# Performance work log

Hardware: AMD Instinct MI355X
Metric: run time of the kernel (lower is better)

Reference implementation:

```python
import jax, jax.numpy as jnp
import numpy as np

H = 16
HD = 128
ROPE_BASE = 10000.0

def _rope_cos_sin(T, dtype):
    inv_freq = 1.0 / (ROPE_BASE ** (jnp.arange(0, HD, 2, dtype=jnp.float32) / HD))  # [HD/2]
    pos = jnp.arange(T, dtype=jnp.float32)
    freqs = pos[:, None] * inv_freq[None, :]  # [T, HD/2]
    return jnp.cos(freqs).astype(dtype), jnp.sin(freqs).astype(dtype)

def _apply_rotary(x, cos, sin):
    # x: [B,H,T,HD]; cos/sin: [T,HD/2]
    x1, x2 = x[..., : HD // 2], x[..., HD // 2 :]
    c = cos[None, None, :, :]
    s = sin[None, None, :, :]
    return jnp.concatenate([x1 * c - x2 * s, x1 * s + x2 * c], axis=-1)

def setup_inputs() -> dict:
    key = jax.random.key(0)
    ks = jax.random.split(key, 5)
    B, T, D = 2, 2048, 2048
    x = jax.random.normal(ks[0], (B, T, D), dtype=jnp.float32)
    Wqkv = jax.random.normal(ks[1], (3 * D, D), dtype=jnp.float32) * (D ** -0.5)
    bqkv = jax.random.normal(ks[2], (3 * D,), dtype=jnp.float32) * 0.02
    Wo = jax.random.normal(ks[3], (D, D), dtype=jnp.float32) * (D ** -0.5)
    bo = jax.random.normal(ks[4], (D,), dtype=jnp.float32) * 0.02
    # causal mask: True = masked (future positions)
    mask = jnp.triu(jnp.ones((T, T), dtype=bool), k=1)[None, None, :, :]
    return {"x": x, "Wqkv": Wqkv, "bqkv": bqkv, "Wo": Wo, "bo": bo, "mask": mask}

def reference(x, Wqkv, bqkv, Wo, bo, mask):
    B, T, D = x.shape
    qkv = x @ Wqkv.T + bqkv  # [B,T,3D]
    q, k, v = jnp.split(qkv, 3, axis=-1)
    def to_heads(t):
        return t.reshape(B, T, H, HD).transpose(0, 2, 1, 3)  # [B,H,T,HD]
    q, k, v = to_heads(q), to_heads(k), to_heads(v)
    cos, sin = _rope_cos_sin(T, x.dtype)
    q = _apply_rotary(q, cos, sin)
    k = _apply_rotary(k, cos, sin)
    scale = HD ** 0.5
    attn = jnp.einsum('bhqd,bhkd->bhqk', q, k) / scale
    neg = -jnp.finfo(x.dtype).max
    attn = jnp.where(mask, neg, attn)
    w = jax.nn.softmax(attn, axis=-1)
    out = jnp.einsum('bhqk,bhkd->bhqd', w, v)  # [B,H,T,HD]
    out = out.transpose(0, 2, 1, 3).reshape(B, T, H * HD)
    return out @ Wo.T + bo
```

## Files before the change

kernel.cpp:

```cpp
#include <hip/hip_runtime.h>
#include <hip/hip_bf16.h>
#include <cstdint>

typedef __bf16 bf16;
typedef __bf16 bf16x8 __attribute__((ext_vector_type(8)));
typedef float  f32x4  __attribute__((ext_vector_type(4)));

#define B_   2
#define T_   2048
#define D_   2048
#define H_   16
#define HD_  128

typedef __attribute__((address_space(3))) void       lds_void;
typedef __attribute__((address_space(1))) const void gbl_void;
__device__ __forceinline__ void glds16(const bf16* g, bf16* l) {
    __builtin_amdgcn_global_load_lds((gbl_void*)g, (lds_void*)l, 16, 0, 0);
}

__device__ __forceinline__ ushort4 cvt4(const float4 v) {
    union { bf16 h[4]; ushort4 u; } pk;
    pk.h[0] = (bf16)v.x; pk.h[1] = (bf16)v.y;
    pk.h[2] = (bf16)v.z; pk.h[3] = (bf16)v.w;
    return pk.u;
}

__global__ __launch_bounds__(256) void convert_xw_kernel(
    const float* __restrict__ x, const float* __restrict__ wqkv,
    bf16* __restrict__ xb, bf16* __restrict__ wqkvb)
{
    const int NX = (B_ * T_ * D_) / 4;
    const int NT = NX + (3 * D_ * D_) / 4;
    for (int g = blockIdx.x * blockDim.x + threadIdx.x; g < NT;
         g += gridDim.x * blockDim.x) {
        if (g < NX) ((ushort4*)xb)[g]      = cvt4(((const float4*)x)[g]);
        else        ((ushort4*)wqkvb)[g-NX] = cvt4(((const float4*)wqkv)[g-NX]);
    }
}

__global__ __launch_bounds__(256) void convert_wo_kernel(
    const float* __restrict__ wo, bf16* __restrict__ wob)
{
    const int N = (D_ * D_) / 4;
    for (int g = blockIdx.x * blockDim.x + threadIdx.x; g < N;
         g += gridDim.x * blockDim.x)
        ((ushort4*)wob)[g] = cvt4(((const float4*)wo)[g]);
}

__device__ __forceinline__ void gemm_core_glds(
    const bf16* __restrict__ A, const bf16* __restrict__ W, int K,
    int bm, int bn, int tid, f32x4 (&acc)[4][4],
    bf16* lds_a, bf16* lds_b)
{
    const int lane = tid & 63, quad = lane >> 4, lcol = lane & 15;
    const int wave = tid >> 6;
    const int wm = (wave >> 1) * 64, wn2 = (wave & 1) * 32;
    const int sw = lcol & 7;
    const int sr = tid >> 3, pc = tid & 7;
    const int sc = (pc ^ (sr & 7)) * 8;
    const bf16* abase = A + (size_t)(bm * 128 + sr) * K + sc;
    const bf16* bbase = W + (size_t)(bn * 128 + sr) * K + sc;
    bf16* la = lds_a + sr * 64 + pc * 8;
    bf16* lb = lds_b + sr * 64 + pc * 8;

    for (int k0 = 0; k0 < K; k0 += 64) {
        __syncthreads();
#pragma unroll
        for (int p = 0; p < 4; p++) {
            glds16(abase + k0 + (size_t)32 * p * K, la + 2048 * p);
            glds16(bbase + k0 + (size_t)32 * p * K, lb + 2048 * p);
        }
        __syncthreads();
#pragma unroll
        for (int kk = 0; kk < 2; kk++) {
            bf16x8 af[4], bfr[4];
#pragma unroll
            for (int i = 0; i < 4; i++)
                af[i] = *(const bf16x8*)&lds_a[(wm + i * 16 + lcol) * 64 +
                                               (((kk * 4 + quad) ^ sw) * 8)];
#pragma unroll
            for (int j = 0; j < 4; j++) {
                const int row = wn2 + (j & 1) * 16 + (j >> 1) * 64 + lcol;
                bfr[j] = *(const bf16x8*)&lds_b[row * 64 +
                                                (((kk * 4 + quad) ^ sw) * 8)];
            }
#pragma unroll
            for (int i = 0; i < 4; i++)
#pragma unroll
                for (int j = 0; j < 4; j++)
                    acc[i][j] = __builtin_amdgcn_mfma_f32_16x16x32_bf16(af[i], bfr[j], acc[i][j], 0, 0, 0);
        }
    }
}

__global__ __launch_bounds__(256) void qkv_gemm_kernel(
    const bf16* __restrict__ xb, const bf16* __restrict__ wqkvb,
    const float* __restrict__ bias,
    bf16* __restrict__ qh, bf16* __restrict__ kh, bf16* __restrict__ vT)
{
    __shared__ bf16 lds_a[128 * 64];
    __shared__ bf16 lds_b[128 * 64];
    const int tid = threadIdx.x;
    const int bm = blockIdx.y, bn = blockIdx.x;
    const int lane = tid & 63, quad = lane >> 4, lcol = lane & 15;
    const int wave = tid >> 6;
    const int wm = (wave >> 1) * 64, wn2 = (wave & 1) * 32;

    f32x4 acc[4][4];
    const f32x4 z = {0.f, 0.f, 0.f, 0.f};
#pragma unroll
    for (int i = 0; i < 4; i++)
#pragma unroll
        for (int j = 0; j < 4; j++) acc[i][j] = z;

    gemm_core_glds(xb, wqkvb, D_, bm, bn, tid, acc, lds_a, lds_b);

    const int n0 = bn * 128;
    const int part = bn / 16;
    const int h = bn & 15;
    const int mb0 = bm * 128 + wm;

    if (part < 2) {
        bf16* dst = (part == 0) ? qh : kh;
#pragma unroll
        for (int i = 0; i < 4; i++) {
#pragma unroll
            for (int jp = 0; jp < 2; jp++) {
                const int d1 = wn2 + jp * 16 + lcol;
                const float invf = __expf(-0.14391156831212787f * (float)d1);
                const float b1 = bias[n0 + d1];
                const float b2 = bias[n0 + d1 + 64];
#pragma unroll
                for (int r = 0; r < 4; r++) {
                    const int m = mb0 + i * 16 + quad * 4 + r;
                    const int bb = m >> 11, t = m & (T_ - 1);
                    const float x1 = acc[i][jp][r] + b1;
                    const float x2 = acc[i][jp + 2][r] + b2;
                    float s, c;
                    __sincosf((float)t * invf, &s, &c);
                    const size_t rowo = ((size_t)(bb * H_ + h) * T_ + t) * HD_;
                    dst[rowo + d1]      = (bf16)(x1 * c - x2 * s);
                    dst[rowo + d1 + 64] = (bf16)(x1 * s + x2 * c);
                }
            }
        }
    } else {
        const int bb = mb0 >> 11, t64 = mb0 & (T_ - 1);
        const int bh = bb * H_ + h;
#pragma unroll
        for (int j = 0; j < 4; j++) {
            const int d = wn2 + (j & 1) * 16 + (j >> 1) * 64 + lcol;
            const float bv = bias[n0 + d];
            bf16* vdst = &vT[((size_t)bh * HD_ + d) * T_ + t64];
#pragma unroll
            for (int r = 0; r < 4; r++) {
                union { bf16 hh[4]; ushort4 u; } pk;
#pragma unroll
                for (int i = 0; i < 4; i++) pk.hh[i] = (bf16)(acc[i][j][r] + bv);
                *(ushort4*)&vdst[(quad * 4 + r) * 4] = pk.u;
            }
        }
    }
}

__global__ __launch_bounds__(256) void attn_kernel(
    const bf16* __restrict__ qh, const bf16* __restrict__ kh,
    const bf16* __restrict__ vT, bf16* __restrict__ ctx)
{
    __shared__ bf16 lds_k[2][64 * 128];
    __shared__ bf16 lds_v[2][128 * 64];
    __shared__ bf16 lds_p[64 * 64];
    const int tid = threadIdx.x;
    const int id = blockIdx.x;
    const int bh = id & 31;
    const int qp = id >> 5;
    const int qtA = 31 - qp;
    const int qtB = qp;
    const int ktA = qtA + 1;
    const int lane = tid & 63, quad = lane >> 4, lcol = lane & 15;
    const int wave = tid >> 6;
    const int wq0 = wave * 16;
    const float scale2 = 0.08838834764831845f * 1.4426950408889634f;
    const int b = bh >> 4, h = bh & 15;

    const bf16* kbase = kh + (size_t)bh * T_ * HD_;
    const bf16* vbase = vT + (size_t)bh * HD_ * T_;

    const int ksrow = tid >> 4;
    const bf16* kstage = kbase + (size_t)ksrow * HD_ + (((tid & 15) ^ ksrow) << 3);
    const int vsd = tid >> 3;
    const bf16* vstage = vbase + (size_t)vsd * T_ + (((tid & 7) ^ (vsd & 7)) << 3);

    int qt_cur = qtA;
    int q0 = qtA * 64;

    bf16x8 qf[4];
    auto load_q = [&](int q0_) {
#pragma unroll
        for (int kk = 0; kk < 4; kk++)
            qf[kk] = *(const bf16x8*)&qh[((size_t)bh * T_ + q0_ + wq0 + lcol) * HD_ +
                                         kk * 32 + quad * 8];
    };
    load_q(q0);

    f32x4 o[8];
    const f32x4 z = {0.f, 0.f, 0.f, 0.f};
#pragma unroll
    for (int jd = 0; jd < 8; jd++) o[jd] = z;
    float l_part[4] = {0.f, 0.f, 0.f, 0.f};

    auto do_epilogue = [&](int q0_) {
        float inv_l[4];
#pragma unroll
        for (int r = 0; r < 4; r++) {
            float rs = l_part[r];
#pragma unroll
            for (int off = 1; off < 16; off <<= 1)
                rs += __shfl_xor(rs, off);
            inv_l[r] = 1.0f / rs;
        }
#pragma unroll
        for (int r = 0; r < 4; r++) {
            const int t = q0_ + wq0 + quad * 4 + r;
#pragma unroll
            for (int jd = 0; jd < 8; jd++)
                ctx[((size_t)(b * T_ + t)) * D_ + h * HD_ + jd * 16 + lcol] =
                    (bf16)(o[jd][r] * inv_l[r]);
        }
    };

#pragma unroll
    for (int p = 0; p < 4; p++) {
        glds16(kstage + (size_t)16 * p * HD_, &lds_k[0][tid * 8 + p * 2048]);
        glds16(vstage + (size_t)32 * p * T_, &lds_v[0][tid * 8 + p * 2048]);
    }

    for (int s = 0; s < 33; s++) {
        __syncthreads();
        if (s + 1 < 33) {
            const int kn = (s + 1 < ktA) ? (s + 1) : (s + 1 - ktA);
            const bf16* ks = kstage + (size_t)kn * 64 * HD_;
            const bf16* vs = vstage + kn * 64;
            bf16* lkd = &lds_k[(s + 1) & 1][tid * 8];
            bf16* lvd = &lds_v[(s + 1) & 1][tid * 8];
#pragma unroll
            for (int p = 0; p < 4; p++) {
                glds16(ks + (size_t)16 * p * HD_, lkd + p * 2048);
                glds16(vs + (size_t)32 * p * T_, lvd + p * 2048);
            }
        }
        if (s == ktA) {
            do_epilogue(q0);
            qt_cur = qtB;
            q0 = qtB * 64;
            load_q(q0);
#pragma unroll
            for (int jd = 0; jd < 8; jd++) o[jd] = z;
#pragma unroll
            for (int r = 0; r < 4; r++) l_part[r] = 0.f;
        }
        const int kt = (s < ktA) ? s : (s - ktA);
        const bf16* lk = lds_k[s & 1];
        const bf16* lv = lds_v[s & 1];

        f32x4 s_acc[4];
#pragma unroll
        for (int j = 0; j < 4; j++) s_acc[j] = z;
        __builtin_amdgcn_s_setprio(1);
#pragma unroll
        for (int kk = 0; kk < 4; kk++) {
#pragma unroll
            for (int j = 0; j < 4; j++) {
                const bf16x8 bk = *(const bf16x8*)&lk[(j * 16 + lcol) * 128 +
                                        (((kk * 4 + quad) ^ lcol) << 3)];
                s_acc[j] = __builtin_amdgcn_mfma_f32_16x16x32_bf16(qf[kk], bk, s_acc[j], 0, 0, 0);
            }
        }
        __builtin_amdgcn_s_setprio(0);

        const bool diag = (kt == qt_cur);
#pragma unroll
        for (int r = 0; r < 4; r++) {
            const int prow = wq0 + quad * 4 + r;
            const int qrow = q0 + prow;
            union { bf16 hh[4]; ushort4 u; } pk;
            float lp = 0.f;
#pragma unroll
            for (int j = 0; j < 4; j++) {
                float p = exp2f(fmaf(s_acc[j][r], scale2, -16.0f));
                if (diag) {
                    const int kcol = kt * 64 + j * 16 + lcol;
                    p = (kcol > qrow) ? 0.f : p;
                }
                lp += p;
                pk.hh[j] = (bf16)p;
            }
            l_part[r] += lp;
            *(ushort4*)&lds_p[prow * 64 + ((lcol * 4) ^ ((prow & 7) << 3))] = pk.u;
        }

#pragma unroll
        for (int kk2 = 0; kk2 < 2; kk2++) {
            const int prow = wq0 + lcol;
            const bf16x8 pf = *(const bf16x8*)&lds_p[prow * 64 +
                                  ((kk2 * 32 + quad * 8) ^ ((lcol & 7) << 3))];
            bf16x8 vf[8];
#pragma unroll
            for (int jd = 0; jd < 8; jd++) {
                const int d = jd * 16 + lcol;
                vf[jd] = *(const bf16x8*)&lv[d * 64 +
                              (((kk2 * 4 + quad) ^ (lcol & 7)) << 3)];
            }
            __builtin_amdgcn_s_setprio(1);
#pragma unroll
            for (int jd = 0; jd < 8; jd++)
                o[jd] = __builtin_amdgcn_mfma_f32_16x16x32_bf16(pf, vf[jd], o[jd], 0, 0, 0);
            __builtin_amdgcn_s_setprio(0);
        }
    }

    do_epilogue(q0);
}

__global__ __launch_bounds__(256) void proj_gemm_kernel(
    const bf16* __restrict__ ctx, const bf16* __restrict__ wob,
    const float* __restrict__ bias, float* __restrict__ out)
{
    __shared__ bf16 lds_a[128 * 64];
    __shared__ bf16 lds_b[128 * 64];
    const int tid = threadIdx.x;
    const int bm = blockIdx.y, bn = blockIdx.x;
    const int lane = tid & 63, quad = lane >> 4, lcol = lane & 15;
    const int wave = tid >> 6;
    const int wm = (wave >> 1) * 64, wn2 = (wave & 1) * 32;

    f32x4 acc[4][4];
    const f32x4 z = {0.f, 0.f, 0.f, 0.f};
#pragma unroll
    for (int i = 0; i < 4; i++)
#pragma unroll
        for (int j = 0; j < 4; j++) acc[i][j] = z;

    gemm_core_glds(ctx, wob, D_, bm, bn, tid, acc, lds_a, lds_b);

    const int n0 = bn * 128;
#pragma unroll
    for (int i = 0; i < 4; i++) {
#pragma unroll
        for (int j = 0; j < 4; j++) {
            const int n = n0 + wn2 + (j & 1) * 16 + (j >> 1) * 64 + lcol;
            const float bv = bias[n];
#pragma unroll
            for (int r = 0; r < 4; r++) {
                const int m = bm * 128 + wm + i * 16 + quad * 4 + r;
                out[(size_t)m * D_ + n] = acc[i][j][r] + bv;
            }
        }
    }
}

extern "C" void kernel_launch(void* const* d_in, const int* in_sizes, int n_in,
                              void* d_out, int out_size, void* d_ws, size_t ws_size,
                              hipStream_t stream)
{
    const float* x    = (const float*)d_in[0];
    const float* Wqkv = (const float*)d_in[1];
    const float* bqkv = (const float*)d_in[2];
    const float* Wo   = (const float*)d_in[3];
    const float* bo   = (const float*)d_in[4];
    float* out = (float*)d_out;

    const size_t HT = (size_t)B_ * H_ * T_ * HD_;
    bf16* xb   = (bf16*)d_ws;
    bf16* qh   = xb + HT;
    bf16* kh   = qh + HT;
    bf16* vT   = kh + HT;
    bf16* ctx  = xb;
    bf16* wob  = qh;
    bf16* wqkvb = (bf16*)d_out;

    convert_xw_kernel<<<2560, 256, 0, stream>>>(x, Wqkv, xb, wqkvb);
    qkv_gemm_kernel<<<dim3(48, 32), 256, 0, stream>>>(xb, wqkvb, bqkv, qh, kh, vT);
    attn_kernel<<<512, 256, 0, stream>>>(qh, kh, vT, ctx);
    convert_wo_kernel<<<1024, 256, 0, stream>>>(Wo, wob);
    proj_gemm_kernel<<<dim3(16, 32), 256, 0, stream>>>(ctx, wob, bo, out);
}
```

Before: 354.6 us.

## Enlarge QKV GEMM tile to 256x256 with 8 waves and double-buffered LDS pipeline

The QKV projection GEMM moves from 128x128 tiles with 4 waves to 256x256 tiles with 8 waves, each wave computing a 64x128 sub-tile. It uses a 128KB double-buffered LDS ring fed by global_load_lds, with split prefetch stages interleaved between barriers and MFMA priority raised. The aim is more operand reuse per byte loaded and loads overlapping with MFMA work. In exchange it uses far more LDS and registers (128 fp32 accumulators per lane) and launches only 384 blocks, which lowers occupancy and may leave some CUs underused.

```diff
diff --git a/kernel.cpp b/kernel.cpp
--- a/kernel.cpp
+++ b/kernel.cpp
@@ -93,70 +93,155 @@
     }
 }
 
-__global__ __launch_bounds__(256) void qkv_gemm_kernel(
+__global__ __launch_bounds__(512, 2) void qkv_gemm_kernel(
     const bf16* __restrict__ xb, const bf16* __restrict__ wqkvb,
     const float* __restrict__ bias,
     bf16* __restrict__ qh, bf16* __restrict__ kh, bf16* __restrict__ vT)
 {
-    __shared__ bf16 lds_a[128 * 64];
-    __shared__ bf16 lds_b[128 * 64];
+    __shared__ bf16 lds[8 * 8192];
     const int tid = threadIdx.x;
-    const int bm = blockIdx.y, bn = blockIdx.x;
+    const int bn = blockIdx.x, bm = blockIdx.y;
     const int lane = tid & 63, quad = lane >> 4, lcol = lane & 15;
     const int wave = tid >> 6;
-    const int wm = (wave >> 1) * 64, wn2 = (wave & 1) * 32;
-
-    f32x4 acc[4][4];
+    const int wm = wave >> 1;
+    const int wn = wave & 1;
+    const int swz = lcol & 7;
+
+    const int sr = tid >> 3, sc = tid & 7;
+    const bf16* ga = xb    + (size_t)(bm * 256 + sr) * D_ + ((sc ^ (sr & 7)) << 3);
+    const bf16* gb = wqkvb + (size_t)(bn * 256 + sr) * D_ + ((sc ^ (sr & 7)) << 3);
+    bf16* ldst = lds + tid * 8;
+
+    auto stage = [&](int t, int kind) {
+        const bf16* g = ((kind & 2) ? gb : ga) +
+                        (size_t)(kind & 1) * 128 * D_ + t * 64;
+        bf16* d = ldst + (((t & 1) * 4 + kind) & 7) * 8192;
+        glds16(g, d);
+        glds16(g + (size_t)64 * D_, d + 4096);
+    };
+
+    f32x4 acc[4][8];
     const f32x4 z = {0.f, 0.f, 0.f, 0.f};
 #pragma unroll
     for (int i = 0; i < 4; i++)
 #pragma unroll
-        for (int j = 0; j < 4; j++) acc[i][j] = z;
-
-    gemm_core_glds(xb, wqkvb, D_, bm, bn, tid, acc, lds_a, lds_b);
-
-    const int n0 = bn * 128;
-    const int part = bn / 16;
-    const int h = bn & 15;
-    const int mb0 = bm * 128 + wm;
+        for (int j = 0; j < 8; j++) acc[i][j] = z;
+
+    const int NT = D_ / 64;
+
+    stage(0, 0); stage(0, 1); stage(0, 2); stage(0, 3);
+    stage(1, 0); stage(1, 1);
+
+#define QKV_TILE(t, par, LASTV)                                                \
+    {                                                                          \
+        if (LASTV) asm volatile("s_waitcnt vmcnt(0)" ::: "memory");            \
+        else       asm volatile("s_waitcnt vmcnt(4)" ::: "memory");            \
+        __builtin_amdgcn_s_barrier();                                          \
+        __builtin_amdgcn_sched_barrier(0);                                     \
+        if ((t) + 1 < NT) { stage((t) + 1, 2); stage((t) + 1, 3); }            \
+        const bf16* sA = lds + ((par) + (wm >> 1)) * 8192 + ((wm & 1) * 64) * 64; \
+        const bf16* sB = lds + ((par) + 2 + wn) * 8192;                        \
+        bf16x8 af[4][2];                                                       \
+        _Pragma("unroll")                                                      \
+        for (int i = 0; i < 4; i++)                                            \
+            _Pragma("unroll")                                                  \
+            for (int kk = 0; kk < 2; kk++)                                     \
+                af[i][kk] = *(const bf16x8*)&sA[(i * 16 + lcol) * 64 +         \
+                                                (((kk * 4 + quad) ^ swz) << 3)]; \
+        _Pragma("unroll")                                                      \
+        for (int jp = 0; jp < 2; jp++) {                 \
+            bf16x8 bf[2][2];                                                   \
+            _Pragma("unroll")                                                  \
+            for (int jj = 0; jj < 2; jj++)                                     \
+                _Pragma("unroll")                                              \
+                for (int kk = 0; kk < 2; kk++)                                 \
+                    bf[jj][kk] = *(const bf16x8*)&sB[((jp * 2 + jj) * 16 + lcol) * 64 + \
+                                                     (((kk * 4 + quad) ^ swz) << 3)]; \
+            __builtin_amdgcn_s_setprio(1);                                     \
+            _Pragma("unroll")                                                  \
+            for (int jj = 0; jj < 2; jj++)                                     \
+                _Pragma("unroll")                                              \
+                for (int kk = 0; kk < 2; kk++)                                 \
+                    _Pragma("unroll")                                          \
+                    for (int i = 0; i < 4; i++)                                \
+                        acc[i][jp * 2 + jj] = __builtin_amdgcn_mfma_f32_16x16x32_bf16( \
+                            af[i][kk], bf[jj][kk], acc[i][jp * 2 + jj], 0, 0, 0); \
+            __builtin_amdgcn_s_setprio(0);                                     \
+        }                                                                      \
+        __builtin_amdgcn_s_barrier();     \
+        __builtin_amdgcn_sched_barrier(0);                                     \
+        if ((t) + 2 < NT) { stage((t) + 2, 0); stage((t) + 2, 1); }            \
+        _Pragma("unroll")                                                      \
+        for (int jp = 2; jp < 4; jp++) {                 \
+            bf16x8 bf[2][2];                                                   \
+            _Pragma("unroll")                                                  \
+            for (int jj = 0; jj < 2; jj++)                                     \
+                _Pragma("unroll")                                              \
+                for (int kk = 0; kk < 2; kk++)                                 \
+                    bf[jj][kk] = *(const bf16x8*)&sB[((jp * 2 + jj) * 16 + lcol) * 64 + \
+                                                     (((kk * 4 + quad) ^ swz) << 3)]; \
+            __builtin_amdgcn_s_setprio(1);                                     \
+            _Pragma("unroll")                                                  \
+            for (int jj = 0; jj < 2; jj++)                                     \
+                _Pragma("unroll")                                              \
+                for (int kk = 0; kk < 2; kk++)                                 \
+                    _Pragma("unroll")                                          \
+                    for (int i = 0; i < 4; i++)                                \
+                        acc[i][jp * 2 + jj] = __builtin_amdgcn_mfma_f32_16x16x32_bf16( \
+                            af[i][kk], bf[jj][kk], acc[i][jp * 2 + jj], 0, 0, 0); \
+            __builtin_amdgcn_s_setprio(0);                                     \
+        }                                                                      \
+    }
+
+    for (int tt = 0; tt < 15; tt++) {
+        QKV_TILE(2 * tt, 0, false);
+        QKV_TILE(2 * tt + 1, 4, false);
+    }
+    QKV_TILE(30, 0, false);
+    QKV_TILE(31, 4, true);
+#undef QKV_TILE
+
+    const int n0 = bn * 256 + wn * 128;
+    const int part = bn >> 3;
+    const int hh = (bn & 7) * 2 + wn;
+    const int mb0 = bm * 256 + wm * 64;
+    const int bb = mb0 >> 11, tb = mb0 & (T_ - 1);
 
     if (part < 2) {
         bf16* dst = (part == 0) ? qh : kh;
 #pragma unroll
-        for (int i = 0; i < 4; i++) {
-#pragma unroll
-            for (int jp = 0; jp < 2; jp++) {
-                const int d1 = wn2 + jp * 16 + lcol;
-                const float invf = __expf(-0.14391156831212787f * (float)d1);
-                const float b1 = bias[n0 + d1];
-                const float b2 = bias[n0 + d1 + 64];
+        for (int jp = 0; jp < 4; jp++) {
+            const int d1 = jp * 16 + lcol;
+            const float invf = __expf(-0.14391156831212787f * (float)d1);
+            const float b1 = bias[n0 + d1];
+            const float b2 = bias[n0 + d1 + 64];
+#pragma unroll
+            for (int i = 0; i < 4; i++) {
 #pragma unroll
                 for (int r = 0; r < 4; r++) {
-                    const int m = mb0 + i * 16 + quad * 4 + r;
-                    const int bb = m >> 11, t = m & (T_ - 1);
+                    const int t = tb + i * 16 + quad * 4 + r;
                     const float x1 = acc[i][jp][r] + b1;
-                    const float x2 = acc[i][jp + 2][r] + b2;
+                    const float x2 = acc[i][jp + 4][r] + b2;
                     float s, c;
                     __sincosf((float)t * invf, &s, &c);
-                    const size_t rowo = ((size_t)(bb * H_ + h) * T_ + t) * HD_;
+                    const size_t rowo = ((size_t)(bb * H_ + hh) * T_ + t) * HD_;
                     dst[rowo + d1]      = (bf16)(x1 * c - x2 * s);
                     dst[rowo + d1 + 64] = (bf16)(x1 * s + x2 * c);
                 }
             }
         }
     } else {
-        const int bb = mb0 >> 11, t64 = mb0 & (T_ - 1);
-        const int bh = bb * H_ + h;
-#pragma unroll
-        for (int j = 0; j < 4; j++) {
-            const int d = wn2 + (j & 1) * 16 + (j >> 1) * 64 + lcol;
+        const int bh = bb * H_ + hh;
+#pragma unroll
+        for (int j = 0; j < 8; j++) {
+            const int d = j * 16 + lcol;
             const float bv = bias[n0 + d];
-            bf16* vdst = &vT[((size_t)bh * HD_ + d) * T_ + t64];
+            bf16* vdst = &vT[((size_t)bh * HD_ + d) * T_ + tb];
 #pragma unroll
             for (int r = 0; r < 4; r++) {
-                union { bf16 hh[4]; ushort4 u; } pk;
-#pragma unroll
-                for (int i = 0; i < 4; i++) pk.hh[i] = (bf16)(acc[i][j][r] + bv);
+                union { bf16 hhv[4]; ushort4 u; } pk;
+#pragma unroll
+                for (int i = 0; i < 4; i++) pk.hhv[i] = (bf16)(acc[i][j][r] + bv);
                 *(ushort4*)&vdst[(quad * 4 + r) * 4] = pk.u;
             }
         }
@@ -380,7 +465,7 @@
     bf16* wqkvb = (bf16*)d_out;
 
     convert_xw_kernel<<<2560, 256, 0, stream>>>(x, Wqkv, xb, wqkvb);
-    qkv_gemm_kernel<<<dim3(48, 32), 256, 0, stream>>>(xb, wqkvb, bqkv, qh, kh, vT);
+    qkv_gemm_kernel<<<dim3(24, 16), 512, 0, stream>>>(xb, wqkvb, bqkv, qh, kh, vT);
     attn_kernel<<<512, 256, 0, stream>>>(qh, kh, vT, ctx);
     convert_wo_kernel<<<1024, 256, 0, stream>>>(Wo, wob);
     proj_gemm_kernel<<<dim3(16, 32), 256, 0, stream>>>(ctx, wob, bo, out);
```

Result: slower. 367.6 us (+3.7%).
